# Kernel optimization log

Hardware: AMD Instinct MI355X
Metric: run time of the kernel (lower is better)

## Reference

```python
import jax, jax.numpy as jnp
import numpy as np
from jax import lax

N_POINTS = 4096
D_FEAT = 64


def setup_inputs() -> dict:
    key = jax.random.key(0)
    x = jax.random.normal(key, (N_POINTS, D_FEAT), dtype=jnp.float32)
    return {"x": x}


def _pairwise_dist(x):
    # Euclidean distance matrix [n, n]; diagonal masked to +inf so a point
    # never pairs with itself. Diagonal of D2 is set to 1.0 (not 0) before
    # sqrt so the backward pass is NaN-free.
    sq = jnp.sum(x * x, axis=1)
    D2 = sq[:, None] + sq[None, :] - 2.0 * (x @ x.T)
    n = x.shape[0]
    eye = jnp.eye(n, dtype=bool)
    D2 = jnp.where(eye, 1.0, jnp.maximum(D2, 1e-12))
    D = jnp.sqrt(D2)
    return jnp.where(eye, jnp.inf, D)


def _h0_flag_diagram(D):
    # Dim-0 persistence of the Rips (flag) filtration: every vertex is born at
    # filtration value 0; the n-1 finite deaths are exactly the edge lengths of
    # the minimum spanning tree of the distance graph. Computed with Prim's
    # algorithm vectorized over the frontier (one lax.scan step per MST edge).
    n = D.shape[0]
    intree0 = jnp.zeros((n,), dtype=bool).at[0].set(True)
    mind0 = D[0]  # min distance from the tree to each vertex

    def step(carry, _):
        mind, intree = carry
        masked = jnp.where(intree, jnp.inf, mind)
        j = jnp.argmin(masked)          # next vertex merged into the tree
        death = masked[j]               # edge length at which its class dies
        intree = intree.at[j].set(True)
        mind = jnp.minimum(mind, D[j])
        return (mind, intree), death

    _, deaths = lax.scan(step, (mind0, intree0), None, length=n - 1)
    births = jnp.zeros_like(deaths)
    return jnp.stack([births, deaths], axis=1)  # [n-1, 2]


def reference(x):
    D = _pairwise_dist(x)
    dgm0 = _h0_flag_diagram(D)
    return dgm0
```

## Files before the change

kernel.cpp:

```cpp
#include <hip/hip_runtime.h>
#include <math.h>


#define N 4096
#define DF 64
#define INF __builtin_huge_valf()

__global__ __launch_bounds__(256) void build_d_kernel(const float* __restrict__ x,
                                                      float* __restrict__ D,
                                                      unsigned long long* __restrict__ best) {
    __shared__ float As[64][68];
    __shared__ float Bs[64][68];
    const int bi = blockIdx.y * 64;
    const int bj = blockIdx.x * 64;
    const int t = threadIdx.x;

#pragma unroll
    for (int g = 0; g < 4; ++g) {
        int idx = t + 256 * g;
        int row = idx >> 4;
        int k4 = (idx & 15) << 2;
        *(float4*)(&As[row][k4]) = *(const float4*)(x + (size_t)(bi + row) * DF + k4);
        *(float4*)(&Bs[row][k4]) = *(const float4*)(x + (size_t)(bj + row) * DF + k4);
    }
    __syncthreads();

    const int ti = (t >> 4) << 2;
    const int tj = (t & 15) << 2;
    float acc[4][4];
#pragma unroll
    for (int r = 0; r < 4; ++r)
#pragma unroll
        for (int c = 0; c < 4; ++c) acc[r][c] = 0.0f;

    for (int k = 0; k < 64; k += 4) {
        float4 a[4], b[4];
#pragma unroll
        for (int r = 0; r < 4; ++r) a[r] = *(const float4*)(&As[ti + r][k]);
#pragma unroll
        for (int c = 0; c < 4; ++c) b[c] = *(const float4*)(&Bs[tj + c][k]);
#pragma unroll
        for (int r = 0; r < 4; ++r)
#pragma unroll
            for (int c = 0; c < 4; ++c) {
                float d0 = a[r].x - b[c].x;
                float d1 = a[r].y - b[c].y;
                float d2 = a[r].z - b[c].z;
                float d3 = a[r].w - b[c].w;
                float s = acc[r][c];
                s = fmaf(d0, d0, s);
                s = fmaf(d1, d1, s);
                s = fmaf(d2, d2, s);
                s = fmaf(d3, d3, s);
                acc[r][c] = s;
            }
    }
#pragma unroll
    for (int r = 0; r < 4; ++r) {
        int i = bi + ti + r;
        float4 v;
        float* vp = &v.x;
        unsigned long long mk = ~0ULL;
#pragma unroll
        for (int c = 0; c < 4; ++c) {
            int j = bj + tj + c;
            vp[c] = (i == j) ? INF : sqrtf(fmaxf(acc[r][c], 1e-12f));
            unsigned long long key =
                ((unsigned long long)__float_as_uint(vp[c]) << 24) |
                ((unsigned long long)(unsigned)i << 12) | (unsigned)j;
            mk = key < mk ? key : mk;
        }
        *(float4*)(D + (size_t)i * N + (bj + tj)) = v;
#pragma unroll
        for (int m = 1; m < 16; m <<= 1) {
            unsigned long long o = __shfl_xor(mk, m, 64);
            mk = o < mk ? o : mk;
        }
        if ((t & 15) == 0) atomicMin(&best[i], mk);
    }
}

__global__ __launch_bounds__(256) void init_kernel(unsigned* comp,
                                                   unsigned long long* best,
                                                   unsigned* nedges, unsigned* done) {
    int i = blockIdx.x * 256 + threadIdx.x;
    if (i < N) {
        comp[i] = (unsigned)i;
        best[i] = ~0ULL;
    }
    if (i == 0) { *nedges = 0u; *done = 0u; }
}

__global__ __launch_bounds__(256) void minedge_d_kernel(const float* __restrict__ D,
                                                        const unsigned* __restrict__ comp,
                                                        unsigned long long* __restrict__ best,
                                                        const unsigned* __restrict__ done) {
    if (*done) return;
    __shared__ unsigned compc[N];
    __shared__ unsigned long long keybuf[256];
    const int t = threadIdx.x;
    const int b = blockIdx.x;
    const int r = t >> 4;
    const int j = t & 15;
    const int rowv = b * 16 + r;

    for (int v = t; v < N; v += 256) compc[v] = comp[v];
    __syncthreads();
    const unsigned cr = compc[rowv];
    const float4* rowp = (const float4*)(D + (size_t)rowv * N);
    unsigned long long mykey = ~0ULL;
#pragma unroll 4
    for (int k = 0; k < 64; ++k) {
        float4 v4 = rowp[j + 16 * k];
        int c0 = 4 * (j + 16 * k);
        const float* vp = &v4.x;
#pragma unroll
        for (int q = 0; q < 4; ++q) {
            int c = c0 + q;
            if (compc[c] != cr) {
                unsigned long long key =
                    ((unsigned long long)__float_as_uint(vp[q]) << 24) |
                    ((unsigned long long)(unsigned)rowv << 12) | (unsigned)c;
                mykey = key < mykey ? key : mykey;
            }
        }
    }
    keybuf[t] = mykey;
    __syncthreads();
    if (t < 16) {
        unsigned long long k = ~0ULL;
#pragma unroll
        for (int i = 0; i < 16; ++i) {
            unsigned long long v2 = keybuf[t * 16 + i];
            k = v2 < k ? v2 : k;
        }
        if (k != ~0ULL) atomicMin(&best[compc[b * 16 + t]], k);
    }
}

__global__ __launch_bounds__(256) void minedge_kernel(const float* __restrict__ x,
                                                      const unsigned* __restrict__ comp,
                                                      unsigned long long* __restrict__ best,
                                                      const unsigned* __restrict__ done) {
    if (*done) return;
    __shared__ float xr[16][64];
    __shared__ float xc[64][68];
    __shared__ unsigned compr[16];
    __shared__ unsigned compc[64];
    __shared__ unsigned long long keybuf[256];
    const int t = threadIdx.x;
    const int b = blockIdx.x;
    const int r = t >> 4;
    const int rowv = b * 16 + r;

    {
        int row = t >> 4, f4 = t & 15;
        *(float4*)&xr[row][f4 * 4] =
            *(const float4*)(x + (size_t)(b * 16 + row) * DF + f4 * 4);
        if (t < 16) compr[t] = comp[b * 16 + t];
    }
    __syncthreads();
    const unsigned cr = compr[r];
    unsigned long long mykey = ~0ULL;

    for (int tile = 0; tile < 64; ++tile) {
        {
#pragma unroll
            for (int q = 0; q < 4; ++q) {
                int idx = t + 256 * q;
                int col = idx >> 4, k4 = (idx & 15) * 4;
                *(float4*)&xc[col][k4] =
                    *(const float4*)(x + (size_t)(tile * 64 + col) * DF + k4);
            }
            if (t < 64) compc[t] = comp[tile * 64 + t];
        }
        __syncthreads();
#pragma unroll
        for (int q = 0; q < 4; ++q) {
            int c = (t & 15) + 16 * q;
            unsigned cc = compc[c];
            if (cc != cr) {
                float s = 0.0f;
#pragma unroll
                for (int k = 0; k < 64; k += 4) {
                    float4 a = *(const float4*)&xr[r][k];
                    float4 bb = *(const float4*)&xc[c][k];
                    float d0 = a.x - bb.x;
                    float d1 = a.y - bb.y;
                    float d2 = a.z - bb.z;
                    float d3 = a.w - bb.w;
                    s = fmaf(d0, d0, s);
                    s = fmaf(d1, d1, s);
                    s = fmaf(d2, d2, s);
                    s = fmaf(d3, d3, s);
                }
                float w = sqrtf(fmaxf(s, 1e-12f));
                unsigned long long key =
                    ((unsigned long long)__float_as_uint(w) << 24) |
                    ((unsigned long long)(unsigned)rowv << 12) |
                    (unsigned)(tile * 64 + c);
                mykey = key < mykey ? key : mykey;
            }
        }
        __syncthreads();
    }
    keybuf[t] = mykey;
    __syncthreads();
    if (t < 16) {
        unsigned long long k = ~0ULL;
#pragma unroll
        for (int i = 0; i < 16; ++i) {
            unsigned long long v2 = keybuf[t * 16 + i];
            k = v2 < k ? v2 : k;
        }
        if (k != ~0ULL) atomicMin(&best[compr[t]], k);
    }
}

__global__ void merge_kernel(unsigned* comp, unsigned long long* best,
                             unsigned long long* edges, unsigned* nedges,
                             unsigned* done) {
    if (*done) return;
    __shared__ unsigned cl[N];
    __shared__ unsigned np[N];
    __shared__ unsigned cnt;
    const int t = threadIdx.x;
    const int bs = blockDim.x;
    for (int v = t; v < N; v += bs) cl[v] = comp[v];
    __syncthreads();
    for (int v = t; v < N; v += bs) {
        unsigned p;
        if (cl[v] == (unsigned)v) {
            unsigned long long k = best[v];
            p = (k != ~0ULL) ? cl[(unsigned)(k & 0xFFFu)] : (unsigned)v;
        } else {
            p = cl[v];
        }
        np[v] = p;
    }
    __syncthreads();
    for (int v = t; v < N; v += bs) {
        if (cl[v] == (unsigned)v) {
            unsigned p = np[v];
            if (p != (unsigned)v) {
                bool mutual = (np[p] == (unsigned)v);
                if (mutual && (unsigned)v < p) {
                    np[v] = (unsigned)v;
                } else {
                    unsigned idx = atomicAdd(nedges, 1u);
                    edges[idx] = best[v];
                }
            }
        }
    }
    __syncthreads();
    for (int it = 0; it < 12; ++it) {
        for (int v = t; v < N; v += bs) np[v] = np[np[v]];
        __syncthreads();
    }
    if (t == 0) cnt = 0;
    __syncthreads();
    unsigned local = 0;
    for (int v = t; v < N; v += bs) {
        comp[v] = np[v];
        best[v] = ~0ULL;
        if (np[v] == (unsigned)v) ++local;
    }
    atomicAdd(&cnt, local);
    __syncthreads();
    if (t == 0 && cnt == 1u) *done = 1u;
}

__global__ __launch_bounds__(1024) void replay_kernel(
        const unsigned long long* __restrict__ edges,
        const unsigned* __restrict__ nedges, float* __restrict__ out) {
    __shared__ __align__(16) unsigned char pool[156680];
    __shared__ unsigned chg;
    unsigned* off = (unsigned*)(pool + 65536);
    unsigned long long* ent = (unsigned long long*)(pool + 0);
    unsigned short* par = (unsigned short*)(pool + 81928);
    unsigned* keyw = (unsigned*)(pool + 90120);
    unsigned long long* key64 = (unsigned long long*)(pool + 0);
    unsigned long long* order = (unsigned long long*)(pool + 0);
    unsigned* ptr = (unsigned*)(pool + 106504);
    unsigned short* rankA = (unsigned short*)(pool + 106504);
    unsigned short* nxtA = (unsigned short*)(pool + 122888);
    unsigned short* twin = (unsigned short*)(pool + 139272);
    unsigned* Sa = (unsigned*)(pool + 32768);
    unsigned* Sb = (unsigned*)(pool + 49152);
    unsigned* T = (unsigned*)(pool + 65536);
    unsigned* vA = (unsigned*)(pool + 122888);
    unsigned* jA = (unsigned*)(pool + 139272);
    unsigned* vB = (unsigned*)(pool + 0);
    unsigned* jB = (unsigned*)(pool + 16384);
    unsigned* csum = (unsigned*)(pool + 155656);
    const int t = threadIdx.x;
    const unsigned ne = *nedges;
    const int ns = 2 * (int)ne;

    for (int v = t; v < N; v += 1024) off[v] = 0u;
    if (t == 0) off[N] = 0u;
    for (int k = t; k < N - 1; k += 1024) out[2 * k] = 0.0f;
    __syncthreads();
    for (int e = t; e < (int)ne; e += 1024) {
        unsigned long long k = edges[e];
        atomicAdd(&off[(unsigned)(k >> 12) & 0xFFFu], 1u);
        atomicAdd(&off[(unsigned)k & 0xFFFu], 1u);
    }
    __syncthreads();
    unsigned sloc = 0;
    unsigned loc[16];
    if (t < 256) {
        int base = t * 16;
#pragma unroll
        for (int i = 0; i < 16; ++i) {
            unsigned d = off[base + i];
            loc[i] = sloc;
            sloc += d;
        }
        csum[t] = sloc;
    }
    __syncthreads();
    for (int d = 1; d < 256; d <<= 1) {
        unsigned addv = 0;
        if (t < 256 && t >= d) addv = csum[t - d];
        __syncthreads();
        if (t < 256) csum[t] += addv;
        __syncthreads();
    }
    if (t < 256) {
        int base = t * 16;
        unsigned excl = csum[t] - sloc;
#pragma unroll
        for (int i = 0; i < 16; ++i) {
            unsigned o = loc[i] + excl;
            off[base + i] = o;
            keyw[base + i] = o;
        }
        if (t == 255) off[N] = csum[255];
    }
    __syncthreads();
    for (int e = t; e < (int)ne; e += 1024) {
        unsigned long long k = edges[e];
        unsigned a = (unsigned)(k >> 12) & 0xFFFu;
        unsigned b = (unsigned)k & 0xFFFu;
        unsigned long long wb = k >> 24;
        unsigned p1 = atomicAdd(&keyw[a], 1u);
        unsigned p2 = atomicAdd(&keyw[b], 1u);
        ent[p1] = (wb << 12) | b;
        ent[p2] = (wb << 12) | a;
        twin[p1] = (unsigned short)p2;
        twin[p2] = (unsigned short)p1;
    }
    __syncthreads();
    const unsigned s0 = off[0];
    for (int s = t; s < ns; s += 1024) {
        unsigned v = (unsigned)ent[s] & 0xFFFu;
        unsigned t2 = twin[s];
        unsigned nx = t2 + 1u;
        if (nx == off[v + 1]) nx = off[v];
        if (nx == s0) nx = 0xFFFFu;
        nxtA[s] = (unsigned short)nx;
        rankA[s] = 1;
    }
    __syncthreads();
    for (int round = 0; round < 13; ++round) {
        unsigned short rr[8], nn[8];
#pragma unroll
        for (int q = 0; q < 8; ++q) {
            int s = t + 1024 * q;
            rr[q] = 0;
            nn[q] = 0xFFFFu;
            if (s < ns) {
                unsigned n2 = nxtA[s];
                if (n2 != 0xFFFFu) {
                    rr[q] = rankA[n2];
                    nn[q] = nxtA[n2];
                }
            }
        }
        __syncthreads();
#pragma unroll
        for (int q = 0; q < 8; ++q) {
            int s = t + 1024 * q;
            if (s < ns && nxtA[s] != 0xFFFFu) {
                rankA[s] = (unsigned short)(rankA[s] + rr[q]);
                nxtA[s] = nn[q];
            }
        }
        __syncthreads();
    }
    for (int s = t; s < ns; s += 1024) {
        unsigned t2 = twin[s];
        if (rankA[s] > rankA[t2]) {
            unsigned v = (unsigned)ent[s] & 0xFFFu;
            par[v] = (unsigned short)((unsigned)ent[t2] & 0xFFFu);
            keyw[v] = (unsigned)(ent[s] >> 12);
        }
    }
    if (t == 0) {
        par[0] = 0;
        chg = 0u;
    }
    __syncthreads();
    for (int v = t; v < N; v += 1024) {
        key64[v] = (v == 0) ? ~0ULL
                            : (((unsigned long long)keyw[v]) << 24) |
                                  ((unsigned long long)par[v] << 12) | (unsigned)v;
    }
    __syncthreads();
    for (int v = t; v < N; v += 1024) ptr[v] = (v == 0) ? 0u : (unsigned)par[v];
    __syncthreads();
    for (;;) {
        for (int v = t; v < N; v += 1024) {
            unsigned p = ptr[v];
            if (key64[p] <= key64[v]) {
                unsigned q = ptr[p];
                if (q != p) {
                    ptr[v] = q;
                    chg = 1u;
                }
            }
        }
        __syncthreads();
        unsigned fin = (chg == 0u);
        __syncthreads();
        if (t == 0) chg = 0u;
        __syncthreads();
        if (fin) break;
    }
    unsigned* Sc = Sa;
    unsigned* Sn = Sb;
    for (int v = t; v < N; v += 1024) Sc[v] = 1u;
    __syncthreads();
    for (int round = 0; round < 64; ++round) {
        for (int v = t; v < N; v += 1024) Sn[v] = 1u;
        __syncthreads();
        for (int v = t; v < N; v += 1024)
            if (v != 0) atomicAdd(&Sn[ptr[v]], Sc[v]);
        __syncthreads();
        for (int v = t; v < N; v += 1024)
            if (Sn[v] != Sc[v]) chg = 1u;
        __syncthreads();
        unsigned fin = (chg == 0u);
        __syncthreads();
        if (t == 0) chg = 0u;
        __syncthreads();
        unsigned* tmp = Sc; Sc = Sn; Sn = tmp;
        if (fin) break;
    }
    for (int v = t; v < N; v += 1024) {
        order[v] = (v == 0)
                       ? (0xFFFFFull << 44)
                       : (((unsigned long long)ptr[v]) << 44) |
                             (((unsigned long long)keyw[v]) << 12) | (unsigned)v;
    }
    __syncthreads();
    for (unsigned k = 2; k <= 4096; k <<= 1) {
        for (unsigned j = k >> 1; j > 0; j >>= 1) {
            for (unsigned i = t; i < 4096; i += 1024) {
                unsigned p = i ^ j;
                if (p > i) {
                    unsigned long long a = order[i], b = order[p];
                    bool up = ((i & k) == 0);
                    if ((a > b) == up) {
                        order[i] = b;
                        order[p] = a;
                    }
                }
            }
            __syncthreads();
        }
    }
    for (int i = t; i < 4096; i += 1024) {
        unsigned vv = (unsigned)order[i] & 0xFFFu;
        T[i] = Sc[vv];
    }
    __syncthreads();
    for (int d = 1; d < 4096; d <<= 1) {
        unsigned addv[4];
#pragma unroll
        for (int q = 0; q < 4; ++q) {
            int i = t + 1024 * q;
            addv[q] = 0;
            if (i >= d && (order[i] >> 44) == (order[i - d] >> 44)) addv[q] = T[i - d];
        }
        __syncthreads();
#pragma unroll
        for (int q = 0; q < 4; ++q) T[t + 1024 * q] += addv[q];
        __syncthreads();
    }
    for (int i = t; i < 4096; i += 1024) {
        unsigned vv = (unsigned)order[i] & 0xFFFu;
        if (vv) {
            vA[vv] = 1u + T[i] - Sc[vv];
            jA[vv] = ptr[vv];
        }
    }
    if (t == 0) {
        vA[0] = 0u;
        jA[0] = 0u;
    }
    __syncthreads();
    {
        unsigned *va = vA, *vb = vB, *ja = jA, *jb = jB;
        for (int r = 0; r < 12; ++r) {
            for (int v = t; v < N; v += 1024) {
                unsigned j2 = ja[v];
                vb[v] = va[v] + va[j2];
                jb[v] = ja[j2];
            }
            __syncthreads();
            unsigned* tmp;
            tmp = va; va = vb; vb = tmp;
            tmp = ja; ja = jb; jb = tmp;
        }
        for (int v = t; v < N; v += 1024) {
            if (v) out[2 * (va[v] - 1) + 1] = __uint_as_float(keyw[v]);
        }
    }
}

extern "C" void kernel_launch(void* const* d_in, const int* in_sizes, int n_in,
                              void* d_out, int out_size, void* d_ws, size_t ws_size,
                              hipStream_t stream) {
    const float* x = (const float*)d_in[0];
    float* out = (float*)d_out;
    const size_t dbytes = (size_t)N * N * 4;

    if (ws_size >= dbytes + 81920) {
        float* D = (float*)d_ws;
        unsigned char* st = (unsigned char*)d_ws + dbytes;
        unsigned long long* best = (unsigned long long*)st;
        unsigned* comp = (unsigned*)(st + 32768);
        unsigned long long* edges = (unsigned long long*)(st + 49152);
        unsigned* nedges = (unsigned*)(st + 81912);
        unsigned* done = (unsigned*)(st + 81916);

        dim3 grid(N / 64, N / 64);
        init_kernel<<<16, 256, 0, stream>>>(comp, best, nedges, done);
        build_d_kernel<<<grid, 256, 0, stream>>>(x, D, best);
        merge_kernel<<<1, 1024, 0, stream>>>(comp, best, edges, nedges, done);
        for (int r = 1; r < 12; ++r) {
            minedge_d_kernel<<<256, 256, 0, stream>>>(D, comp, best, done);
            merge_kernel<<<1, 1024, 0, stream>>>(comp, best, edges, nedges, done);
        }
        replay_kernel<<<1, 1024, 0, stream>>>(edges, nedges, out);
    } else {
        unsigned char* ws = (unsigned char*)d_ws;
        unsigned* comp = (unsigned*)ws;
        unsigned long long* best = (unsigned long long*)(ws + 16384);
        unsigned long long* edges = (unsigned long long*)(ws + 49152);
        unsigned* nedges = (unsigned*)(ws + 81920);
        unsigned* done = (unsigned*)(ws + 81984);

        init_kernel<<<16, 256, 0, stream>>>(comp, best, nedges, done);
        for (int r = 0; r < 12; ++r) {
            minedge_kernel<<<256, 256, 0, stream>>>(x, comp, best, done);
            merge_kernel<<<1, 1024, 0, stream>>>(comp, best, edges, nedges, done);
        }
        replay_kernel<<<1, 1024, 0, stream>>>(edges, nedges, out);
    }
}
```

Measured before the change: 486.4 us.

## Exploit distance symmetry in D build and fuse last bitonic sort stages

The distance kernel now launches only upper-triangular 64x64 tiles (2080 blocks) and writes each off-diagonal tile twice, directly and transposed through shared memory. Column minima are also reduced and atomically merged into best, so the pairwise distance arithmetic is roughly halved. Separately, the bitonic sort in the merge/replay kernel handles the last two strides (j=2,1) in registers per thread, saving two barriers per k stage. In exchange it adds a serial while-loop to decode each block's tile index and more shared memory per block, which may reduce occupancy.

```diff
diff --git a/kernel.cpp b/kernel.cpp
--- a/kernel.cpp
+++ b/kernel.cpp
@@ -11,72 +11,128 @@
                                                       unsigned long long* __restrict__ best) {
     __shared__ float As[64][68];
     __shared__ float Bs[64][68];
-    const int bi = blockIdx.y * 64;
-    const int bj = blockIdx.x * 64;
+    __shared__ float Ts[64][68];
+    __shared__ unsigned long long colbuf[64][16];
     const int t = threadIdx.x;
 
-#pragma unroll
-    for (int g = 0; g < 4; ++g) {
-        int idx = t + 256 * g;
-        int row = idx >> 4;
-        int k4 = (idx & 15) << 2;
-        *(float4*)(&As[row][k4]) = *(const float4*)(x + (size_t)(bi + row) * DF + k4);
-        *(float4*)(&Bs[row][k4]) = *(const float4*)(x + (size_t)(bj + row) * DF + k4);
-    }
-    __syncthreads();
-
-    const int ti = (t >> 4) << 2;
-    const int tj = (t & 15) << 2;
-    float acc[4][4];
-#pragma unroll
-    for (int r = 0; r < 4; ++r)
-#pragma unroll
-        for (int c = 0; c < 4; ++c) acc[r][c] = 0.0f;
-
-    for (int k = 0; k < 64; k += 4) {
-        float4 a[4], b[4];
-#pragma unroll
-        for (int r = 0; r < 4; ++r) a[r] = *(const float4*)(&As[ti + r][k]);
-#pragma unroll
-        for (int c = 0; c < 4; ++c) b[c] = *(const float4*)(&Bs[tj + c][k]);
+    int br = 0;
+    {
+        int rem = blockIdx.x;
+        while (rem >= 64 - br) {
+            rem -= 64 - br;
+            ++br;
+        }
+        br = br;
+        int bc = br + rem;
+        const int bi = br * 64;
+        const int bj = bc * 64;
+
+#pragma unroll
+        for (int g = 0; g < 4; ++g) {
+            int idx = t + 256 * g;
+            int row = idx >> 4;
+            int k4 = (idx & 15) << 2;
+            *(float4*)(&As[row][k4]) =
+                *(const float4*)(x + (size_t)(bi + row) * DF + k4);
+            *(float4*)(&Bs[row][k4]) =
+                *(const float4*)(x + (size_t)(bj + row) * DF + k4);
+        }
+        __syncthreads();
+
+        const int ti = (t >> 4) << 2;
+        const int tj = (t & 15) << 2;
+        float acc[4][4];
 #pragma unroll
         for (int r = 0; r < 4; ++r)
 #pragma unroll
+            for (int c = 0; c < 4; ++c) acc[r][c] = 0.0f;
+
+        for (int k = 0; k < 64; k += 4) {
+            float4 a[4], b[4];
+#pragma unroll
+            for (int r = 0; r < 4; ++r) a[r] = *(const float4*)(&As[ti + r][k]);
+#pragma unroll
+            for (int c = 0; c < 4; ++c) b[c] = *(const float4*)(&Bs[tj + c][k]);
+#pragma unroll
+            for (int r = 0; r < 4; ++r)
+#pragma unroll
+                for (int c = 0; c < 4; ++c) {
+                    float d0 = a[r].x - b[c].x;
+                    float d1 = a[r].y - b[c].y;
+                    float d2 = a[r].z - b[c].z;
+                    float d3 = a[r].w - b[c].w;
+                    float s = acc[r][c];
+                    s = fmaf(d0, d0, s);
+                    s = fmaf(d1, d1, s);
+                    s = fmaf(d2, d2, s);
+                    s = fmaf(d3, d3, s);
+                    acc[r][c] = s;
+                }
+        }
+
+        float val[4][4];
+#pragma unroll
+        for (int r = 0; r < 4; ++r) {
+            int i = bi + ti + r;
+            float4 v;
+            float* vp = &v.x;
+            unsigned long long mk = ~0ULL;
+#pragma unroll
             for (int c = 0; c < 4; ++c) {
-                float d0 = a[r].x - b[c].x;
-                float d1 = a[r].y - b[c].y;
-                float d2 = a[r].z - b[c].z;
-                float d3 = a[r].w - b[c].w;
-                float s = acc[r][c];
-                s = fmaf(d0, d0, s);
-                s = fmaf(d1, d1, s);
-                s = fmaf(d2, d2, s);
-                s = fmaf(d3, d3, s);
-                acc[r][c] = s;
-            }
-    }
-#pragma unroll
-    for (int r = 0; r < 4; ++r) {
-        int i = bi + ti + r;
-        float4 v;
-        float* vp = &v.x;
-        unsigned long long mk = ~0ULL;
-#pragma unroll
-        for (int c = 0; c < 4; ++c) {
-            int j = bj + tj + c;
-            vp[c] = (i == j) ? INF : sqrtf(fmaxf(acc[r][c], 1e-12f));
-            unsigned long long key =
-                ((unsigned long long)__float_as_uint(vp[c]) << 24) |
-                ((unsigned long long)(unsigned)i << 12) | (unsigned)j;
-            mk = key < mk ? key : mk;
-        }
-        *(float4*)(D + (size_t)i * N + (bj + tj)) = v;
-#pragma unroll
-        for (int m = 1; m < 16; m <<= 1) {
-            unsigned long long o = __shfl_xor(mk, m, 64);
-            mk = o < mk ? o : mk;
-        }
-        if ((t & 15) == 0) atomicMin(&best[i], mk);
+                int j = bj + tj + c;
+                float w = (i == j) ? INF : sqrtf(fmaxf(acc[r][c], 1e-12f));
+                val[r][c] = w;
+                vp[c] = w;
+                unsigned long long key =
+                    ((unsigned long long)__float_as_uint(w) << 24) |
+                    ((unsigned long long)(unsigned)i << 12) | (unsigned)j;
+                mk = key < mk ? key : mk;
+            }
+            *(float4*)(D + (size_t)i * N + (bj + tj)) = v;
+#pragma unroll
+            for (int m = 1; m < 16; m <<= 1) {
+                unsigned long long o = __shfl_xor(mk, m, 64);
+                mk = o < mk ? o : mk;
+            }
+            if ((t & 15) == 0) atomicMin(&best[i], mk);
+        }
+
+        if (br != bc) {
+#pragma unroll
+            for (int c = 0; c < 4; ++c) {
+                unsigned long long ck = ~0ULL;
+                int j = bj + tj + c;
+#pragma unroll
+                for (int r = 0; r < 4; ++r) {
+                    int i = bi + ti + r;
+                    float w = val[r][c];
+                    Ts[tj + c][ti + r] = w;
+                    unsigned long long key =
+                        ((unsigned long long)__float_as_uint(w) << 24) |
+                        ((unsigned long long)(unsigned)j << 12) | (unsigned)i;
+                    ck = key < ck ? key : ck;
+                }
+                colbuf[tj + c][t >> 4] = ck;
+            }
+            __syncthreads();
+            {
+                int row = t >> 2;
+                int seg = (t & 3) * 16;
+                float4* dst = (float4*)(D + (size_t)(bj + row) * N + bi + seg);
+#pragma unroll
+                for (int q = 0; q < 4; ++q)
+                    dst[q] = *(const float4*)(&Ts[row][seg + 4 * q]);
+            }
+            if (t < 64) {
+                unsigned long long k = ~0ULL;
+#pragma unroll
+                for (int i2 = 0; i2 < 16; ++i2) {
+                    unsigned long long v2 = colbuf[t][i2];
+                    k = v2 < k ? v2 : k;
+                }
+                atomicMin(&best[bj + t], k);
+            }
+        }
     }
 }
 
@@ -457,7 +513,7 @@
     }
     __syncthreads();
     for (unsigned k = 2; k <= 4096; k <<= 1) {
-        for (unsigned j = k >> 1; j > 0; j >>= 1) {
+        for (unsigned j = k >> 1; j >= 4; j >>= 1) {
             for (unsigned i = t; i < 4096; i += 1024) {
                 unsigned p = i ^ j;
                 if (p > i) {
@@ -471,6 +527,30 @@
             }
             __syncthreads();
         }
+        {
+            int base = 4 * t;
+            unsigned long long e0 = order[base + 0];
+            unsigned long long e1 = order[base + 1];
+            unsigned long long e2 = order[base + 2];
+            unsigned long long e3 = order[base + 3];
+            if (k >= 4) {
+                bool up = (((unsigned)base & k) == 0);
+                unsigned long long tmp;
+                if ((e0 > e2) == up) { tmp = e0; e0 = e2; e2 = tmp; }
+                if ((e1 > e3) == up) { tmp = e1; e1 = e3; e3 = tmp; }
+                if ((e0 > e1) == up) { tmp = e0; e0 = e1; e1 = tmp; }
+                if ((e2 > e3) == up) { tmp = e2; e2 = e3; e3 = tmp; }
+            } else {
+                unsigned long long tmp;
+                if (e0 > e1) { tmp = e0; e0 = e1; e1 = tmp; }
+                if (e2 < e3) { tmp = e2; e2 = e3; e3 = tmp; }
+            }
+            order[base + 0] = e0;
+            order[base + 1] = e1;
+            order[base + 2] = e2;
+            order[base + 3] = e3;
+            __syncthreads();
+        }
     }
     for (int i = t; i < 4096; i += 1024) {
         unsigned vv = (unsigned)order[i] & 0xFFFu;
@@ -537,9 +617,8 @@
         unsigned* nedges = (unsigned*)(st + 81912);
         unsigned* done = (unsigned*)(st + 81916);
 
-        dim3 grid(N / 64, N / 64);
         init_kernel<<<16, 256, 0, stream>>>(comp, best, nedges, done);
-        build_d_kernel<<<grid, 256, 0, stream>>>(x, D, best);
+        build_d_kernel<<<2080, 256, 0, stream>>>(x, D, best);
         merge_kernel<<<1, 1024, 0, stream>>>(comp, best, edges, nedges, done);
         for (int r = 1; r < 12; ++r) {
             minedge_d_kernel<<<256, 256, 0, stream>>>(D, comp, best, done);
```

New measurement: 472.6 us. 1.03x faster.
